# Optimization experiments

Measured on AMD Instinct MI355X. Metric: run time of the kernel, lower is better.

## Reference

```python
import jax, jax.numpy as jnp
import numpy as np

N_TF, N_GENES, W, FANIN, B = 1024, 20000, 4, 16, 128
M = N_GENES * W  # middle width = 80000


def _build_edges(rng):
    # layer 1: each of the M per-gene nodes draws FANIN random TF inputs
    out1 = np.repeat(np.arange(M, dtype=np.int32), FANIN)
    in1 = rng.integers(0, N_TF, size=M * FANIN).astype(np.int32)
    in1[-1] = N_TF - 1  # ensure full input dim is touched
    # layer 2: dense WxW block per gene (node i of gene g sees all W nodes of gene g)
    out2 = np.repeat(np.arange(M, dtype=np.int32), W)
    gene = np.arange(M, dtype=np.int32) // W
    in2 = (gene[:, None] * W + np.arange(W, dtype=np.int32)[None, :]).reshape(-1)
    # layer 3: each gene output sums its W nodes
    out3 = np.repeat(np.arange(N_GENES, dtype=np.int32), W)
    in3 = np.arange(M, dtype=np.int32)
    return out1, in1, out2, in2, out3, in3


def setup_inputs() -> dict:
    key = jax.random.key(0)
    ks = jax.random.split(key, 7)
    rng = np.random.default_rng(0)
    out1, in1, out2, in2, out3, in3 = _build_edges(rng)
    scale1 = 1.0 / np.sqrt(FANIN)
    scale2 = 1.0 / np.sqrt(W)
    return {
        "features": jax.random.normal(ks[0], (B, N_TF), jnp.float32),
        "w1": jax.random.normal(ks[1], (out1.shape[0],), jnp.float32) * scale1,
        "b1": jax.random.normal(ks[2], (M,), jnp.float32) * 0.01,
        "w2": jax.random.normal(ks[3], (out2.shape[0],), jnp.float32) * scale2,
        "b2": jax.random.normal(ks[4], (M,), jnp.float32) * 0.01,
        "w3": jax.random.normal(ks[5], (out3.shape[0],), jnp.float32) * scale2,
        "b3": jax.random.normal(ks[6], (N_GENES,), jnp.float32) * 0.01,
        "out1": jnp.asarray(out1), "in1": jnp.asarray(in1),
        "out2": jnp.asarray(out2), "in2": jnp.asarray(in2),
        "out3": jnp.asarray(out3), "in3": jnp.asarray(in3),
    }


def _sparse_linear(x, w, b, out_idx, in_idx):
    # x: [B, n_in]; per-edge gather-multiply-scatter, y[b, o] = sum_e w_e * x[b, in_e] + b_o
    contrib = x.T[in_idx] * w[:, None]                      # [nnz, B]
    y = jax.ops.segment_sum(contrib, out_idx, num_segments=b.shape[0])  # [n_out, B]
    return y.T + b


def reference(features, w1, b1, w2, b2, w3, b3, out1, in1, out2, in2, out3, in3):
    h = jnp.tanh(_sparse_linear(features, w1, b1, out1, in1))
    h = jnp.tanh(_sparse_linear(h, w2, b2, out2, in2))
    return _sparse_linear(h, w3, b3, out3, in3)  # [B, N_GENES]
```

## Files before the change

kernel.cpp:

```cpp
#include <hip/hip_runtime.h>
#include <hip/hip_bf16.h>

#define N_TF    1024
#define N_GENES 20000
#define WW      4
#define FANIN   16
#define BATCH   128

__device__ __forceinline__ float fast_tanh(float x) {
    float t = __expf(2.0f * x);
    return 1.0f - 2.0f * __builtin_amdgcn_rcpf(t + 1.0f);
}

__global__ __launch_bounds__(256) void transpose_kernel(
    const float* __restrict__ in, float* __restrict__ out)
{
    __shared__ float tile[32][33];
    const int bx = blockIdx.x;
    const int by = blockIdx.y;
    const int tx = threadIdx.x;
    const int ty = threadIdx.y;
#pragma unroll
    for (int k = 0; k < 32; k += 8)
        tile[ty + k][tx] = in[(by * 32 + ty + k) * N_TF + bx * 32 + tx];
    __syncthreads();
#pragma unroll
    for (int k = 0; k < 32; k += 8)
        out[(bx * 32 + ty + k) * BATCH + by * 32 + tx] = tile[tx][ty + k];
}

constexpr int GENES_PER_BLOCK = 16;
constexpr int GENES_PER_WAVE  = 4;
constexpr int YPAD            = 130;

__global__ __launch_bounds__(256) void fused_kernel(
    const float* __restrict__ xT,
    const float* __restrict__ w1,
    const float* __restrict__ b1,
    const int*   __restrict__ in1,
    const float* __restrict__ w2,
    const float* __restrict__ b2,
    const float* __restrict__ w3,
    const float* __restrict__ b3,
    float*       __restrict__ out)
{
    __shared__ float ytile[GENES_PER_BLOCK * YPAD];

    const int tid  = threadIdx.x;
    const int wid  = __builtin_amdgcn_readfirstlane(tid >> 6);
    const int lane = tid & 63;
    const int g_base = blockIdx.x * GENES_PER_BLOCK + wid * GENES_PER_WAVE;
    const float2* __restrict__ xT2 = (const float2*)xT;

    for (int gi = 0; gi < GENES_PER_WAVE; ++gi) {
        const int g = g_base + gi;

        float2 h1[WW];
#pragma unroll
        for (int i = 0; i < WW; ++i) {
            const int o = g * WW + i;
            const int ebase = o * FANIN;
            float ax = 0.0f, ay = 0.0f;
#pragma unroll
            for (int j = 0; j < FANIN; ++j) {
                const float w   = w1[ebase + j];
                const int   idx = in1[ebase + j];
                const float2 xv = xT2[idx * (BATCH / 2) + lane];
                ax += w * xv.x;
                ay += w * xv.y;
            }
            const float bb = b1[o];
            h1[i].x = fast_tanh(ax + bb);
            h1[i].y = fast_tanh(ay + bb);
        }

        float2 h2[WW];
#pragma unroll
        for (int i = 0; i < WW; ++i) {
            const int o = g * WW + i;
            float sx = b2[o], sy = sx;
#pragma unroll
            for (int k = 0; k < WW; ++k) {
                const float w = w2[o * WW + k];
                sx += w * h1[k].x;
                sy += w * h1[k].y;
            }
            h2[i].x = fast_tanh(sx);
            h2[i].y = fast_tanh(sy);
        }

        float yx = b3[g], yy = yx;
#pragma unroll
        for (int i = 0; i < WW; ++i) {
            const float w = w3[g * WW + i];
            yx += w * h2[i].x;
            yy += w * h2[i].y;
        }

        const int gl = wid * GENES_PER_WAVE + gi;
        ytile[gl * YPAD + 2 * lane]     = yx;
        ytile[gl * YPAD + 2 * lane + 1] = yy;
    }

    __syncthreads();

    const int g0 = blockIdx.x * GENES_PER_BLOCK;
#pragma unroll
    for (int it = 0; it < (GENES_PER_BLOCK * BATCH) / 256; ++it) {
        const int idx = it * 256 + tid;
        const int gl  = idx & (GENES_PER_BLOCK - 1);
        const int b   = idx >> 4;
        out[b * N_GENES + g0 + gl] = ytile[gl * YPAD + b];
    }
}

extern "C" void kernel_launch(void* const* d_in, const int* in_sizes, int n_in,
                              void* d_out, int out_size, void* d_ws, size_t ws_size,
                              hipStream_t stream)
{
    const float* features = (const float*)d_in[0];
    const float* w1 = (const float*)d_in[1];
    const float* b1 = (const float*)d_in[2];
    const float* w2 = (const float*)d_in[3];
    const float* b2 = (const float*)d_in[4];
    const float* w3 = (const float*)d_in[5];
    const float* b3 = (const float*)d_in[6];
    const int*   in1 = (const int*)d_in[8];
    float* out = (float*)d_out;

    float* xT = (float*)d_ws;

    hipLaunchKernelGGL(transpose_kernel, dim3(32, 4), dim3(32, 8), 0, stream,
                       features, xT);
    hipLaunchKernelGGL(fused_kernel, dim3(N_GENES / GENES_PER_BLOCK), dim3(256), 0, stream,
                       xT, w1, b1, in1, w2, b2, w3, b3, out);
}
```

Measured before the change: 134.8 us.

## Run layer-1 gather-FMA in packed fp16 with pre-packed weights

```diff
diff --git a/kernel.cpp b/kernel.cpp
--- a/kernel.cpp
+++ b/kernel.cpp
@@ -1,19 +1,23 @@
 #include <hip/hip_runtime.h>
-#include <hip/hip_bf16.h>
+#include <hip/hip_fp16.h>
 
 #define N_TF    1024
 #define N_GENES 20000
 #define WW      4
 #define FANIN   16
 #define BATCH   128
+#define MM      (N_GENES * WW)
+#define NNZ1    (MM * FANIN)
+
+typedef unsigned int uint32;
 
 __device__ __forceinline__ float fast_tanh(float x) {
     float t = __expf(2.0f * x);
     return 1.0f - 2.0f * __builtin_amdgcn_rcpf(t + 1.0f);
 }
 
-__global__ __launch_bounds__(256) void transpose_kernel(
-    const float* __restrict__ in, float* __restrict__ out)
+__global__ __launch_bounds__(256) void transpose_cvt_kernel(
+    const float* __restrict__ in, __half* __restrict__ out)
 {
     __shared__ float tile[32][33];
     const int bx = blockIdx.x;
@@ -26,23 +30,37 @@
     __syncthreads();
 #pragma unroll
     for (int k = 0; k < 32; k += 8)
-        out[(bx * 32 + ty + k) * BATCH + by * 32 + tx] = tile[tx][ty + k];
+        out[(bx * 32 + ty + k) * BATCH + by * 32 + tx] =
+            __float2half(tile[tx][ty + k]);
 }
 
-constexpr int GENES_PER_BLOCK = 16;
-constexpr int GENES_PER_WAVE  = 4;
+__global__ __launch_bounds__(256) void pack_w1_kernel(
+    const float* __restrict__ w1, uint32* __restrict__ w1d)
+{
+    const int i = blockIdx.x * 256 + threadIdx.x;
+    if (i < NNZ1) {
+        __half h = __float2half(w1[i]);
+        uint32 u = (uint32)__half_as_ushort(h);
+        w1d[i] = (u << 16) | u;
+    }
+}
+
+constexpr int GENES_PER_BLOCK = 8;
+constexpr int GENES_PER_WAVE  = 2;
 constexpr int YPAD            = 130;
 
+template <bool PACKW>
 __global__ __launch_bounds__(256) void fused_kernel(
-    const float* __restrict__ xT,
-    const float* __restrict__ w1,
-    const float* __restrict__ b1,
-    const int*   __restrict__ in1,
-    const float* __restrict__ w2,
-    const float* __restrict__ b2,
-    const float* __restrict__ w3,
-    const float* __restrict__ b3,
-    float*       __restrict__ out)
+    const __half* __restrict__ xh,
+    const uint32* __restrict__ w1d,
+    const float*  __restrict__ w1,
+    const float*  __restrict__ b1,
+    const int*    __restrict__ in1,
+    const float*  __restrict__ w2,
+    const float*  __restrict__ b2,
+    const float*  __restrict__ w3,
+    const float*  __restrict__ b3,
+    float*        __restrict__ out)
 {
     __shared__ float ytile[GENES_PER_BLOCK * YPAD];
 
@@ -50,8 +68,9 @@
     const int wid  = __builtin_amdgcn_readfirstlane(tid >> 6);
     const int lane = tid & 63;
     const int g_base = blockIdx.x * GENES_PER_BLOCK + wid * GENES_PER_WAVE;
-    const float2* __restrict__ xT2 = (const float2*)xT;
+    const __half2* __restrict__ xc = (const __half2*)xh;
 
+#pragma unroll
     for (int gi = 0; gi < GENES_PER_WAVE; ++gi) {
         const int g = g_base + gi;
 
@@ -60,18 +79,24 @@
         for (int i = 0; i < WW; ++i) {
             const int o = g * WW + i;
             const int ebase = o * FANIN;
-            float ax = 0.0f, ay = 0.0f;
+            __half2 acc = __half2half2(__ushort_as_half((unsigned short)0));
 #pragma unroll
             for (int j = 0; j < FANIN; ++j) {
-                const float w   = w1[ebase + j];
-                const int   idx = in1[ebase + j];
-                const float2 xv = xT2[idx * (BATCH / 2) + lane];
-                ax += w * xv.x;
-                ay += w * xv.y;
+                const int idx = in1[ebase + j];
+                const __half2 xv = xc[idx * (BATCH / 2) + lane];
+                __half2 wv;
+                if (PACKW) {
+                    const uint32 wd = w1d[ebase + j];
+                    wv = *reinterpret_cast<const __half2*>(&wd);
+                } else {
+                    wv = __half2half2(__float2half(w1[ebase + j]));
+                }
+                acc = __hfma2(wv, xv, acc);
             }
-            const float bb = b1[o];
-            h1[i].x = fast_tanh(ax + bb);
-            h1[i].y = fast_tanh(ay + bb);
+            const float2 af = __half22float2(acc);
+            const float  bb = b1[o];
+            h1[i].x = fast_tanh(af.x + bb);
+            h1[i].y = fast_tanh(af.y + bb);
         }
 
         float2 h2[WW];
@@ -109,7 +134,7 @@
     for (int it = 0; it < (GENES_PER_BLOCK * BATCH) / 256; ++it) {
         const int idx = it * 256 + tid;
         const int gl  = idx & (GENES_PER_BLOCK - 1);
-        const int b   = idx >> 4;
+        const int b   = idx >> 3;
         out[b * N_GENES + g0 + gl] = ytile[gl * YPAD + b];
     }
 }
@@ -128,10 +153,23 @@
     const int*   in1 = (const int*)d_in[8];
     float* out = (float*)d_out;
 
-    float* xT = (float*)d_ws;
+    const size_t w1d_bytes = (size_t)NNZ1 * sizeof(uint32);
+    const size_t xh_bytes  = (size_t)N_TF * BATCH * sizeof(__half);
+    uint32* w1d = (uint32*)d_ws;
+    const bool packw = ws_size >= w1d_bytes + xh_bytes;
+    __half* xh = packw ? (__half*)((char*)d_ws + w1d_bytes) : (__half*)d_ws;
 
-    hipLaunchKernelGGL(transpose_kernel, dim3(32, 4), dim3(32, 8), 0, stream,
-                       features, xT);
-    hipLaunchKernelGGL(fused_kernel, dim3(N_GENES / GENES_PER_BLOCK), dim3(256), 0, stream,
-                       xT, w1, b1, in1, w2, b2, w3, b3, out);
+    hipLaunchKernelGGL(transpose_cvt_kernel, dim3(32, 4), dim3(32, 8), 0, stream,
+                       features, xh);
+    if (packw) {
+        hipLaunchKernelGGL(pack_w1_kernel, dim3((NNZ1 + 255) / 256), dim3(256), 0,
+                           stream, w1, w1d);
+        hipLaunchKernelGGL((fused_kernel<true>), dim3(N_GENES / GENES_PER_BLOCK),
+                           dim3(256), 0, stream,
+                           xh, w1d, w1, b1, in1, w2, b2, w3, b3, out);
+    } else {
+        hipLaunchKernelGGL((fused_kernel<false>), dim3(N_GENES / GENES_PER_BLOCK),
+                           dim3(256), 0, stream,
+                           xh, (const uint32*)nullptr, w1, b1, in1, w2, b2, w3, b3, out);
+    }
 }
```

Result: faster. 117.3 us (-13.0%).

## Stage fp16 transposed features in LDS and split batch across block pairs

Applied to the files above, without the earlier changes.

```diff
diff --git a/kernel.cpp b/kernel.cpp
--- a/kernel.cpp
+++ b/kernel.cpp
@@ -1,19 +1,32 @@
 #include <hip/hip_runtime.h>
-#include <hip/hip_bf16.h>
+#include <hip/hip_fp16.h>
 
 #define N_TF    1024
 #define N_GENES 20000
 #define WW      4
 #define FANIN   16
 #define BATCH   128
+#define HALF_B  64
+#define MM      (N_GENES * WW)
+#define NNZ1    (MM * FANIN)
+
+#define NCHUNK   128
+#define NBLK     (NCHUNK * 2)
+#define NTHREADS 1024
+#define NWAVES   16
+#define MAXG     160
+#define YPADE    68
+#define XH_BYTES (N_TF * HALF_B * 2)
+#define YT_BYTES (MAXG * YPADE * 2)
+#define LDS_BYTES (XH_BYTES + YT_BYTES)
 
 __device__ __forceinline__ float fast_tanh(float x) {
     float t = __expf(2.0f * x);
     return 1.0f - 2.0f * __builtin_amdgcn_rcpf(t + 1.0f);
 }
 
-__global__ __launch_bounds__(256) void transpose_kernel(
-    const float* __restrict__ in, float* __restrict__ out)
+__global__ __launch_bounds__(256) void transpose_cvt_kernel(
+    const float* __restrict__ in, __half* __restrict__ out)
 {
     __shared__ float tile[32][33];
     const int bx = blockIdx.x;
@@ -24,93 +37,117 @@
     for (int k = 0; k < 32; k += 8)
         tile[ty + k][tx] = in[(by * 32 + ty + k) * N_TF + bx * 32 + tx];
     __syncthreads();
+    const int b = by * 32 + tx;
+    const int h = b >> 6;
+    const int bl = b & 63;
 #pragma unroll
-    for (int k = 0; k < 32; k += 8)
-        out[(bx * 32 + ty + k) * BATCH + by * 32 + tx] = tile[tx][ty + k];
+    for (int k = 0; k < 32; k += 8) {
+        const int tf = bx * 32 + ty + k;
+        out[h * (N_TF * HALF_B) + tf * HALF_B + bl] = __float2half(tile[tx][ty + k]);
+    }
 }
 
-constexpr int GENES_PER_BLOCK = 16;
-constexpr int GENES_PER_WAVE  = 4;
-constexpr int YPAD            = 130;
+__global__ __launch_bounds__(NTHREADS) void fused_kernel(
+    const __half* __restrict__ xhs,
+    const float*  __restrict__ w1,
+    const float*  __restrict__ b1,
+    const int*    __restrict__ in1,
+    const float*  __restrict__ w2,
+    const float*  __restrict__ b2,
+    const float*  __restrict__ w3,
+    const float*  __restrict__ b3,
+    float*        __restrict__ out)
+{
+    extern __shared__ char smem[];
+    __half* xh = (__half*)smem;
+    __half* yt = (__half*)(smem + XH_BYTES);
 
-__global__ __launch_bounds__(256) void fused_kernel(
-    const float* __restrict__ xT,
-    const float* __restrict__ w1,
-    const float* __restrict__ b1,
-    const int*   __restrict__ in1,
-    const float* __restrict__ w2,
-    const float* __restrict__ b2,
-    const float* __restrict__ w3,
-    const float* __restrict__ b3,
-    float*       __restrict__ out)
-{
-    __shared__ float ytile[GENES_PER_BLOCK * YPAD];
+    const int tid   = threadIdx.x;
+    const int bx    = blockIdx.x;
+    const int h     = bx & 1;
+    const int chunk = bx >> 1;
+    const int g0    = chunk * 156 + (chunk < 32 ? chunk : 32);
+    const int ng    = 156 + (chunk < 32 ? 1 : 0);
+    const int nquad = (ng + 3) >> 2;
 
-    const int tid  = threadIdx.x;
-    const int wid  = __builtin_amdgcn_readfirstlane(tid >> 6);
+    {
+        const uint4* __restrict__ src = (const uint4*)(xhs + h * (N_TF * HALF_B));
+        uint4* dst = (uint4*)xh;
+#pragma unroll
+        for (int i = 0; i < (XH_BYTES / 16) / NTHREADS; ++i)
+            dst[i * NTHREADS + tid] = src[i * NTHREADS + tid];
+    }
+    __syncthreads();
+
+    const int wid  = tid >> 6;
     const int lane = tid & 63;
-    const int g_base = blockIdx.x * GENES_PER_BLOCK + wid * GENES_PER_WAVE;
-    const float2* __restrict__ xT2 = (const float2*)xT;
+    const int q    = lane >> 4;
+    const int li   = lane & 15;
+    const __half2 hzero = __half2half2(__float2half(0.0f));
 
-    for (int gi = 0; gi < GENES_PER_WAVE; ++gi) {
-        const int g = g_base + gi;
-
-        float2 h1[WW];
+    for (int qd = wid; qd < nquad; qd += NWAVES) {
+        const int gl = qd * 4 + q;
+        const int g  = g0 + gl;
+        float h1[WW][4];
 #pragma unroll
         for (int i = 0; i < WW; ++i) {
-            const int o = g * WW + i;
-            const int ebase = o * FANIN;
-            float ax = 0.0f, ay = 0.0f;
+            const int eb = g * 64 + i * 16;
+            __half2 acc0 = hzero, acc1 = hzero;
 #pragma unroll
             for (int j = 0; j < FANIN; ++j) {
-                const float w   = w1[ebase + j];
-                const int   idx = in1[ebase + j];
-                const float2 xv = xT2[idx * (BATCH / 2) + lane];
-                ax += w * xv.x;
-                ay += w * xv.y;
+                const int   e   = eb + j;
+                const int   idx = in1[e];
+                const float wf  = w1[e];
+                const __half2 wd = __half2half2(__float2half(wf));
+                const __half2* xp =
+                    (const __half2*)((const char*)xh + idx * (HALF_B * 2) + li * 8);
+                const __half2 x0 = xp[0];
+                const __half2 x1 = xp[1];
+                acc0 = __hfma2(wd, x0, acc0);
+                acc1 = __hfma2(wd, x1, acc1);
             }
-            const float bb = b1[o];
-            h1[i].x = fast_tanh(ax + bb);
-            h1[i].y = fast_tanh(ay + bb);
+            const float  bb = b1[g * 4 + i];
+            const float2 f0 = __half22float2(acc0);
+            const float2 f1 = __half22float2(acc1);
+            h1[i][0] = fast_tanh(f0.x + bb);
+            h1[i][1] = fast_tanh(f0.y + bb);
+            h1[i][2] = fast_tanh(f1.x + bb);
+            h1[i][3] = fast_tanh(f1.y + bb);
         }
 
-        float2 h2[WW];
+        float h2[WW][4];
 #pragma unroll
         for (int i = 0; i < WW; ++i) {
-            const int o = g * WW + i;
-            float sx = b2[o], sy = sx;
+            const float4 w  = *(const float4*)(w2 + g * 16 + i * 4);
+            const float  bb = b2[g * 4 + i];
 #pragma unroll
-            for (int k = 0; k < WW; ++k) {
-                const float w = w2[o * WW + k];
-                sx += w * h1[k].x;
-                sy += w * h1[k].y;
+            for (int e = 0; e < 4; ++e) {
+                const float s = bb + w.x * h1[0][e] + w.y * h1[1][e]
+                                   + w.z * h1[2][e] + w.w * h1[3][e];
+                h2[i][e] = fast_tanh(s);
             }
-            h2[i].x = fast_tanh(sx);
-            h2[i].y = fast_tanh(sy);
         }
 
-        float yx = b3[g], yy = yx;
+        const float4 wv = *(const float4*)(w3 + g * 4);
+        const float  bv = b3[g];
+        float y[4];
 #pragma unroll
-        for (int i = 0; i < WW; ++i) {
-            const float w = w3[g * WW + i];
-            yx += w * h2[i].x;
-            yy += w * h2[i].y;
+        for (int e = 0; e < 4; ++e)
+            y[e] = bv + wv.x * h2[0][e] + wv.y * h2[1][e]
+                      + wv.z * h2[2][e] + wv.w * h2[3][e];
+
+        if (gl < ng) {
+            __half2* yp = (__half2*)((char*)yt + gl * (YPADE * 2) + li * 8);
+            yp[0] = __floats2half2_rn(y[0], y[1]);
+            yp[1] = __floats2half2_rn(y[2], y[3]);
         }
-
-        const int gl = wid * GENES_PER_WAVE + gi;
-        ytile[gl * YPAD + 2 * lane]     = yx;
-        ytile[gl * YPAD + 2 * lane + 1] = yy;
     }
-
     __syncthreads();
 
-    const int g0 = blockIdx.x * GENES_PER_BLOCK;
-#pragma unroll
-    for (int it = 0; it < (GENES_PER_BLOCK * BATCH) / 256; ++it) {
-        const int idx = it * 256 + tid;
-        const int gl  = idx & (GENES_PER_BLOCK - 1);
-        const int b   = idx >> 4;
-        out[b * N_GENES + g0 + gl] = ytile[gl * YPAD + b];
+    for (int b = wid; b < HALF_B; b += NWAVES) {
+        const int row = (h * HALF_B + b) * N_GENES + g0;
+        for (int gl = lane; gl < ng; gl += 64)
+            out[row + gl] = __half2float(yt[gl * YPADE + b]);
     }
 }
 
@@ -128,10 +165,10 @@
     const int*   in1 = (const int*)d_in[8];
     float* out = (float*)d_out;
 
-    float* xT = (float*)d_ws;
+    __half* xhs = (__half*)d_ws;
 
-    hipLaunchKernelGGL(transpose_kernel, dim3(32, 4), dim3(32, 8), 0, stream,
-                       features, xT);
-    hipLaunchKernelGGL(fused_kernel, dim3(N_GENES / GENES_PER_BLOCK), dim3(256), 0, stream,
-                       xT, w1, b1, in1, w2, b2, w3, b3, out);
+    hipLaunchKernelGGL(transpose_cvt_kernel, dim3(32, 4), dim3(32, 8), 0, stream,
+                       features, xhs);
+    hipLaunchKernelGGL(fused_kernel, dim3(NBLK), dim3(NTHREADS), LDS_BYTES, stream,
+                       xhs, w1, b1, in1, w2, b2, w3, b3, out);
 }
```

After: 128.7 us. 4.5% less time.
